# Kernel tuning notes

Hardware: AMD Instinct MI355X
Metric: run time of the kernel (lower is better)

The kernel has to match this reference:

```python
import jax, jax.numpy as jnp
import numpy as np

N_FEATURES, D_IN, D_OUT = 64, 128, 128
BATCH = 8192

def setup_inputs() -> dict:
    key = jax.random.key(0)
    kx, kw, kb = jax.random.split(key, 3)
    x = jax.random.normal(kx, (BATCH, N_FEATURES, D_IN), dtype=jnp.float32)
    # mimic nn.Linear init: U(-1/sqrt(d_in), 1/sqrt(d_in)) for weight and bias
    bound = 1.0 / np.sqrt(D_IN)
    weight = jax.random.uniform(kw, (N_FEATURES, D_IN, D_OUT), dtype=jnp.float32, minval=-bound, maxval=bound)
    bias = jax.random.uniform(kb, (N_FEATURES, D_OUT), dtype=jnp.float32, minval=-bound, maxval=bound)
    return {"x": x, "weight": weight, "bias": bias}

def reference(x, weight, bias):
    # per-feature linear: [B,F,I] x [F,I,O] -> [B,F,O]; same math as
    # (x[...,None] * weight[None]).sum(-2) + bias[None], expressed as grouped GEMM
    out = jnp.einsum('bfi,fio->bfo', x, weight)
    return out + bias[None]
```

## Files before the change

kernel.cpp:

```cpp
#include <hip/hip_runtime.h>
#include <hip/hip_bf16.h>


#define BATCH 8192
#define NF 64
#define DI 128
#define DO 128
#define BM 128
#define TILES_PER_BLOCK 4
#define CHUNKS (BATCH / BM / TILES_PER_BLOCK)

typedef __attribute__((ext_vector_type(8))) short short8;
typedef __attribute__((ext_vector_type(4))) float floatx4;

static __device__ __forceinline__ unsigned short f2bf(float f) {
    union { float f; unsigned u; } v; v.f = f;
    unsigned r = v.u + 0x7fffu + ((v.u >> 16) & 1u);
    return (unsigned short)(r >> 16);
}

__global__ __launch_bounds__(256, 2)
void nlinear_kernel(const float* __restrict__ x,
                    const float* __restrict__ w,
                    const float* __restrict__ bias,
                    float* __restrict__ out) {
    __shared__ unsigned short lds_x[BM * DI];
    __shared__ unsigned short lds_wt[DO * DI];
    __shared__ float lds_bias[DO];

    int b = blockIdx.x;
    int logical = (b & 7) * (CHUNKS * NF / 8) + (b >> 3);
    int f = logical >> 4;
    int chunk = logical & 15;

    int tid  = threadIdx.x;
    int lane = tid & 63;
    int wid  = tid >> 6;

    const float* wf = w + (size_t)f * DI * DO;
    #pragma unroll 4
    for (int it = 0; it < 16; ++it) {
        int id = it * 256 + tid;
        int i  = id >> 5;
        int o4 = (id & 31) << 2;
        floatx4 v = *(const floatx4*)(wf + i * DO + o4);
        #pragma unroll
        for (int j = 0; j < 4; ++j) {
            int o = o4 + j;
            int byte = o * 256 + ((i * 2) ^ ((o & 7) << 4));
            *(unsigned short*)((char*)lds_wt + byte) = f2bf(v[j]);
        }
    }
    if (tid < DO) lds_bias[tid] = bias[f * DO + tid];

    for (int t = 0; t < TILES_PER_BLOCK; ++t) {
        int row0 = (chunk * TILES_PER_BLOCK + t) * BM;

        __syncthreads();

        #pragma unroll 8
        for (int it = 0; it < 16; ++it) {
            int id = it * 256 + tid;
            int r  = id >> 5;
            int c4 = (id & 31) << 2;
            const float* xp = x + (size_t)(row0 + r) * (NF * DI) + f * DI + c4;
            floatx4 v = *(const floatx4*)xp;
            ushort4 pk;
            pk.x = f2bf(v[0]); pk.y = f2bf(v[1]);
            pk.z = f2bf(v[2]); pk.w = f2bf(v[3]);
            int byte = r * 256 + ((c4 * 2) ^ ((r & 7) << 4));
            *(ushort4*)((char*)lds_x + byte) = pk;
        }

        __syncthreads();

        floatx4 acc[2][8];
        #pragma unroll
        for (int m = 0; m < 2; ++m)
            #pragma unroll
            for (int n = 0; n < 8; ++n)
                acc[m][n] = (floatx4){0.f, 0.f, 0.f, 0.f};

        int lrow = lane & 15;
        int lk16 = (lane >> 4) * 16;

        #pragma unroll
        for (int kk = 0; kk < 4; ++kk) {
            int kbyte = kk * 64 + lk16;
            short8 a[2], bf[8];
            #pragma unroll
            for (int m = 0; m < 2; ++m) {
                int r = wid * 32 + m * 16 + lrow;
                a[m] = *(const short8*)((const char*)lds_x +
                        r * 256 + (kbyte ^ ((r & 7) << 4)));
            }
            #pragma unroll
            for (int n = 0; n < 8; ++n) {
                int o = n * 16 + lrow;
                bf[n] = *(const short8*)((const char*)lds_wt +
                        o * 256 + (kbyte ^ ((o & 7) << 4)));
            }
            #pragma unroll
            for (int m = 0; m < 2; ++m)
                #pragma unroll
                for (int n = 0; n < 8; ++n)
                    acc[m][n] = __builtin_amdgcn_mfma_f32_16x16x32_bf16(
                        a[m], bf[n], acc[m][n], 0, 0, 0);
        }

        int col0 = lane & 15;
        int rgrp = lane >> 4;
        #pragma unroll
        for (int m = 0; m < 2; ++m) {
            int rbase = row0 + wid * 32 + m * 16 + rgrp * 4;
            #pragma unroll
            for (int n = 0; n < 8; ++n) {
                int o = n * 16 + col0;
                float bv = lds_bias[o];
                #pragma unroll
                for (int j = 0; j < 4; ++j) {
                    out[(size_t)(rbase + j) * (NF * DO) + f * DO + o] =
                        acc[m][n][j] + bv;
                }
            }
        }
    }
}

extern "C" void kernel_launch(void* const* d_in, const int* in_sizes, int n_in,
                              void* d_out, int out_size, void* d_ws, size_t ws_size,
                              hipStream_t stream) {
    const float* x    = (const float*)d_in[0];
    const float* wght = (const float*)d_in[1];
    const float* bias = (const float*)d_in[2];
    float* out        = (float*)d_out;

    dim3 grid(NF * CHUNKS);
    dim3 block(256);
    nlinear_kernel<<<grid, block, 0, stream>>>(x, wght, bias, out);
}
```

Measured before the change: 161.4 us.

## Load x straight to registers, swap MFMA operands for vector stores, drop x LDS

```diff
diff --git a/kernel.cpp b/kernel.cpp
--- a/kernel.cpp
+++ b/kernel.cpp
@@ -2,13 +2,13 @@
 #include <hip/hip_bf16.h>
 
 
-#define BATCH 8192
 #define NF 64
 #define DI 128
 #define DO 128
 #define BM 128
-#define TILES_PER_BLOCK 4
-#define CHUNKS (BATCH / BM / TILES_PER_BLOCK)
+#define TILES 4
+#define CHUNKS 16
+#define RS (NF * DI)
 
 typedef __attribute__((ext_vector_type(8))) short short8;
 typedef __attribute__((ext_vector_type(4))) float floatx4;
@@ -19,17 +19,16 @@
     return (unsigned short)(r >> 16);
 }
 
-__global__ __launch_bounds__(256, 2)
+__global__ __launch_bounds__(256, 3)
 void nlinear_kernel(const float* __restrict__ x,
                     const float* __restrict__ w,
                     const float* __restrict__ bias,
                     float* __restrict__ out) {
-    __shared__ unsigned short lds_x[BM * DI];
     __shared__ unsigned short lds_wt[DO * DI];
     __shared__ float lds_bias[DO];
 
     int b = blockIdx.x;
-    int logical = (b & 7) * (CHUNKS * NF / 8) + (b >> 3);
+    int logical = (b & 7) * (NF * CHUNKS / 8) + (b >> 3);
     int f = logical >> 4;
     int chunk = logical & 15;
 
@@ -38,7 +37,7 @@
     int wid  = tid >> 6;
 
     const float* wf = w + (size_t)f * DI * DO;
-    #pragma unroll 4
+    #pragma unroll
     for (int it = 0; it < 16; ++it) {
         int id = it * 256 + tid;
         int i  = id >> 5;
@@ -47,82 +46,67 @@
         #pragma unroll
         for (int j = 0; j < 4; ++j) {
             int o = o4 + j;
-            int byte = o * 256 + ((i * 2) ^ ((o & 7) << 4));
+            int byte = o * 256 + ((i * 2) ^ ((o & 15) << 4));
             *(unsigned short*)((char*)lds_wt + byte) = f2bf(v[j]);
         }
     }
     if (tid < DO) lds_bias[tid] = bias[f * DO + tid];
+    __syncthreads();
 
-    for (int t = 0; t < TILES_PER_BLOCK; ++t) {
-        int row0 = (chunk * TILES_PER_BLOCK + t) * BM;
+    int lrow = lane & 15;
+    int kq   = lane >> 4;
 
-        __syncthreads();
+    floatx4 bias4[8];
+    #pragma unroll
+    for (int n = 0; n < 8; ++n)
+        bias4[n] = *(const floatx4*)(lds_bias + n * 16 + kq * 4);
 
-        #pragma unroll 8
-        for (int it = 0; it < 16; ++it) {
-            int id = it * 256 + tid;
-            int r  = id >> 5;
-            int c4 = (id & 31) << 2;
-            const float* xp = x + (size_t)(row0 + r) * (NF * DI) + f * DI + c4;
-            floatx4 v = *(const floatx4*)xp;
-            ushort4 pk;
-            pk.x = f2bf(v[0]); pk.y = f2bf(v[1]);
-            pk.z = f2bf(v[2]); pk.w = f2bf(v[3]);
-            int byte = r * 256 + ((c4 * 2) ^ ((r & 7) << 4));
-            *(ushort4*)((char*)lds_x + byte) = pk;
-        }
-
-        __syncthreads();
+    for (int t = 0; t < TILES; ++t) {
+        int row0 = (chunk * TILES + t) * BM + wid * 32;
 
         floatx4 acc[2][8];
         #pragma unroll
         for (int m = 0; m < 2; ++m)
             #pragma unroll
             for (int n = 0; n < 8; ++n)
-                acc[m][n] = (floatx4){0.f, 0.f, 0.f, 0.f};
-
-        int lrow = lane & 15;
-        int lk16 = (lane >> 4) * 16;
+                acc[m][n] = bias4[n];
 
         #pragma unroll
         for (int kk = 0; kk < 4; ++kk) {
-            int kbyte = kk * 64 + lk16;
-            short8 a[2], bf[8];
+            short8 ax[2];
             #pragma unroll
             for (int m = 0; m < 2; ++m) {
-                int r = wid * 32 + m * 16 + lrow;
-                a[m] = *(const short8*)((const char*)lds_x +
-                        r * 256 + (kbyte ^ ((r & 7) << 4)));
+                const float* p = x + (size_t)(row0 + m * 16 + lrow) * RS
+                                   + f * DI + kk * 32 + kq * 8;
+                floatx4 v0 = *(const floatx4*)p;
+                floatx4 v1 = *(const floatx4*)(p + 4);
+                short8 a;
+                a[0] = (short)f2bf(v0[0]); a[1] = (short)f2bf(v0[1]);
+                a[2] = (short)f2bf(v0[2]); a[3] = (short)f2bf(v0[3]);
+                a[4] = (short)f2bf(v1[0]); a[5] = (short)f2bf(v1[1]);
+                a[6] = (short)f2bf(v1[2]); a[7] = (short)f2bf(v1[3]);
+                ax[m] = a;
             }
+            int kb = kk * 64 + kq * 16;
             #pragma unroll
             for (int n = 0; n < 8; ++n) {
                 int o = n * 16 + lrow;
-                bf[n] = *(const short8*)((const char*)lds_wt +
-                        o * 256 + (kbyte ^ ((o & 7) << 4)));
+                short8 bw = *(const short8*)((const char*)lds_wt
+                              + o * 256 + (kb ^ ((o & 15) << 4)));
+                acc[0][n] = __builtin_amdgcn_mfma_f32_16x16x32_bf16(
+                                bw, ax[0], acc[0][n], 0, 0, 0);
+                acc[1][n] = __builtin_amdgcn_mfma_f32_16x16x32_bf16(
+                                bw, ax[1], acc[1][n], 0, 0, 0);
             }
-            #pragma unroll
-            for (int m = 0; m < 2; ++m)
-                #pragma unroll
-                for (int n = 0; n < 8; ++n)
-                    acc[m][n] = __builtin_amdgcn_mfma_f32_16x16x32_bf16(
-                        a[m], bf[n], acc[m][n], 0, 0, 0);
         }
 
-        int col0 = lane & 15;
-        int rgrp = lane >> 4;
         #pragma unroll
         for (int m = 0; m < 2; ++m) {
-            int rbase = row0 + wid * 32 + m * 16 + rgrp * 4;
+            float* op = out + (size_t)(row0 + m * 16 + lrow) * RS
+                            + f * DO + kq * 4;
             #pragma unroll
-            for (int n = 0; n < 8; ++n) {
-                int o = n * 16 + col0;
-                float bv = lds_bias[o];
-                #pragma unroll
-                for (int j = 0; j < 4; ++j) {
-                    out[(size_t)(rbase + j) * (NF * DO) + f * DO + o] =
-                        acc[m][n][j] + bv;
-                }
-            }
+            for (int n = 0; n < 8; ++n)
+                *(floatx4*)(op + n * 16) = acc[m][n];
         }
     }
 }
```

Measured after the change: 298.0 us. +84.6%, slower.
